# Optimization experiments

Measured on AMD Instinct MI355X. Metric: run time of the kernel, lower is better.

Reference implementation:

```python
import jax, jax.numpy as jnp
import numpy as np
from jax import lax

D_MODEL = 768
D_STATE = 64
D_CONV = 4
EXPAND = 2
HEADDIM = 64
D_INNER = EXPAND * D_MODEL          # 1536
NHEADS = D_INNER // HEADDIM          # 24
NGROUPS = 1
CONV_DIM = D_INNER + 2 * NGROUPS * D_STATE      # 1664
D_IN_PROJ = 2 * D_INNER + 2 * NGROUPS * D_STATE + NHEADS  # 3224
EPS = 1e-5


def setup_inputs() -> dict:
    key = jax.random.key(0)
    ks = jax.random.split(key, 8)
    B, L = 2, 4096
    x = jax.random.normal(ks[0], (B, L, D_MODEL), jnp.float32)
    W_in = jax.random.normal(ks[1], (D_MODEL, D_IN_PROJ), jnp.float32) * (D_MODEL ** -0.5)
    conv_w = jax.random.normal(ks[2], (CONV_DIM, D_CONV), jnp.float32) * 0.2
    conv_b = jnp.zeros((CONV_DIM,), jnp.float32)
    # dt_bias so that softplus(dt_bias) ~ [1e-3, 1e-1], like mamba init
    dt = jax.random.uniform(ks[3], (NHEADS,), jnp.float32, 1e-3, 1e-1)
    dt_bias = dt + jnp.log(-jnp.expm1(-dt))
    A_log = jnp.log(jax.random.uniform(ks[4], (NHEADS,), jnp.float32, 1.0, 16.0))
    D = jnp.ones((NHEADS,), jnp.float32)
    norm_w = jnp.ones((D_INNER,), jnp.float32)
    W_out = jax.random.normal(ks[5], (D_INNER, D_MODEL), jnp.float32) * (D_INNER ** -0.5)
    return {"x": x, "W_in": W_in, "conv_w": conv_w, "conv_b": conv_b,
            "dt_bias": dt_bias, "A_log": A_log, "D": D,
            "norm_w": norm_w, "W_out": W_out}


def _mamba2(x, W_in, conv_w, conv_b, dt_bias, A_log, D, norm_w, W_out):
    B, L, _ = x.shape
    zxbcdt = x @ W_in                                  # (B,L,3224)
    z = zxbcdt[..., :D_INNER]                          # gate
    xBC = zxbcdt[..., D_INNER:D_INNER + CONV_DIM]
    dt = zxbcdt[..., D_INNER + CONV_DIM:]              # (B,L,H)
    dt = jax.nn.softplus(dt + dt_bias)

    # causal depthwise conv1d, kernel D_CONV, then SiLU
    xp = jnp.pad(xBC, ((0, 0), (D_CONV - 1, 0), (0, 0)))
    conv = sum(xp[:, k:k + L, :] * conv_w[:, k] for k in range(D_CONV))
    xBC = jax.nn.silu(conv + conv_b)

    xs = xBC[..., :D_INNER].reshape(B, L, NHEADS, HEADDIM)
    Bm = xBC[..., D_INNER:D_INNER + D_STATE]           # (B,L,N)
    Cm = xBC[..., D_INNER + D_STATE:]                  # (B,L,N)

    A = -jnp.exp(A_log)                                # (H,)
    dA = jnp.exp(dt * A)                               # (B,L,H)

    def step(h, inp):
        dA_t, dt_t, x_t, B_t, C_t = inp
        # h: (B,H,P,N)
        h = h * dA_t[:, :, None, None] \
            + (dt_t[:, :, None] * x_t)[..., None] * B_t[:, None, None, :]
        y = jnp.einsum('bhpn,bn->bhp', h, C_t)
        return h, y

    inps = (jnp.moveaxis(dA, 1, 0), jnp.moveaxis(dt, 1, 0),
            jnp.moveaxis(xs, 1, 0), jnp.moveaxis(Bm, 1, 0),
            jnp.moveaxis(Cm, 1, 0))
    h0 = jnp.zeros((B, NHEADS, HEADDIM, D_STATE), x.dtype)
    _, ys = lax.scan(step, h0, inps)                   # (L,B,H,P)
    y = jnp.moveaxis(ys, 0, 1) + D[None, None, :, None] * xs
    y = y.reshape(B, L, D_INNER)

    # gated RMSNorm: norm(y * silu(z)) * norm_w
    y = y * jax.nn.silu(z)
    y = y * lax.rsqrt(jnp.mean(y * y, axis=-1, keepdims=True) + EPS) * norm_w
    return y @ W_out


def reference(x, W_in, conv_w, conv_b, dt_bias, A_log, D, norm_w, W_out):
    return _mamba2(x, W_in, conv_w, conv_b, dt_bias, A_log, D, norm_w, W_out)
```

## Files before the change

### kernel.cpp

```cpp
#include <hip/hip_runtime.h>

#define B_   2
#define L_   4096
#define DM   768
#define DI   1536
#define DS   64
#define H_   24
#define P_   64
#define CD   1664
#define NPJ  3224
#define N1   3200
#define Q_   64
#define NC   64
#define SP   76
#define HS   72
#define WDS  772
#define CROWS 16

typedef short          bf16x8 __attribute__((ext_vector_type(8)));
typedef _Float16       f16x8  __attribute__((ext_vector_type(8)));
typedef unsigned short us8    __attribute__((ext_vector_type(8)));
typedef unsigned short us4    __attribute__((ext_vector_type(4)));
typedef float          f32x4  __attribute__((ext_vector_type(4)));

__device__ __forceinline__ unsigned short f2bf(float f) {
  unsigned u = __float_as_uint(f);
  u += 0x7fffu + ((u >> 16) & 1u);
  return (unsigned short)(u >> 16);
}
__device__ __forceinline__ float bf2f(unsigned short u) {
  return __uint_as_float(((unsigned)u) << 16);
}
__device__ __forceinline__ float siluf(float x) { return x / (1.f + expf(-x)); }
__device__ __forceinline__ float softplusf(float x) { return (x > 20.f) ? x : log1pf(expf(x)); }

__device__ __forceinline__ void gload16(const unsigned short* g, unsigned short* l) {
  __builtin_amdgcn_global_load_lds(
      (const __attribute__((address_space(1))) void*)g,
      (__attribute__((address_space(3))) void*)l, 16, 0, 0);
}

__global__ __launch_bounds__(256)
void k_transpose_cast(const float* __restrict__ src, unsigned short* __restrict__ dst,
                      int R, int C)
{
  __shared__ float tile[32][33];
  const int tx = threadIdx.x & 31, ty = threadIdx.x >> 5;
  const int r0 = blockIdx.x * 32, c0 = blockIdx.y * 32;
#pragma unroll
  for (int r = 0; r < 4; ++r) {
    int rr = r0 + ty + r * 8, cc = c0 + tx;
    if (rr < R && cc < C) tile[ty + r * 8][tx] = src[(size_t)rr * C + cc];
  }
  __syncthreads();
#pragma unroll
  for (int r = 0; r < 4; ++r) {
    int orow = c0 + ty + r * 8, ocol = r0 + tx;
    if (orow < C && ocol < R) dst[(size_t)orow * R + ocol] = f2bf(tile[tx][ty + r * 8]);
  }
}

__global__ void k_wdtT(const float* __restrict__ W_in, float* __restrict__ WdtT)
{
  const int idx = blockIdx.x * 256 + threadIdx.x;
  if (idx >= H_ * DM) return;
  const int k = idx / H_, h = idx % H_;
  WdtT[(size_t)h * DM + k] = W_in[(size_t)k * NPJ + N1 + h];
}

template<int BM, int BN, int WM, int WN, bool OUT_BF16>
__global__ __launch_bounds__(256)
void k_gemm_t(const unsigned short* __restrict__ A, const unsigned short* __restrict__ Bt,
              void* __restrict__ C0v, int ld0, int ncol0,
              void* __restrict__ C1v, int ld1, int K)
{
  constexpr int MI = WM / 16, NI = WN / 16;
  constexpr int WAVES_N = BN / WN;
  constexpr int RA = BM / 32, RB = BN / 32;
  const int m0 = blockIdx.x * BM, n0 = blockIdx.y * BN;
  __shared__ unsigned short As[BM][64];
  __shared__ unsigned short Bs[BN][64];
  const int tid  = threadIdx.x;
  const int wave = tid >> 6, lane = tid & 63;
  const int quad = lane >> 4, r16 = lane & 15;
  const int wm = (wave / WAVES_N) * WM, wn = (wave % WAVES_N) * WN;

  const int lr8 = lane >> 3;
  const int csw = ((lane & 7) ^ lr8) * 8;
  const unsigned short* gA = A  + (size_t)(m0 + wave * 8 + lr8) * K + csw;
  const unsigned short* gB = Bt + (size_t)(n0 + wave * 8 + lr8) * K + csw;
  unsigned short* lA = &As[wave * 8][0] + (size_t)lane * 8;
  unsigned short* lB = &Bs[wave * 8][0] + (size_t)lane * 8;

  f32x4 acc[MI][NI];
#pragma unroll
  for (int mi = 0; mi < MI; ++mi)
#pragma unroll
    for (int ni = 0; ni < NI; ++ni) acc[mi][ni] = (f32x4){0.f, 0.f, 0.f, 0.f};

  for (int k0 = 0; k0 < K; k0 += 64) {
#pragma unroll
    for (int r = 0; r < RA; ++r)
      gload16(gA + (size_t)(r * 32) * K + k0, lA + (size_t)r * 32 * 64);
#pragma unroll
    for (int r = 0; r < RB; ++r)
      gload16(gB + (size_t)(r * 32) * K + k0, lB + (size_t)r * 32 * 64);
    __syncthreads();
    bf16x8 af[MI][2], bfr[NI][2];
#pragma unroll
    for (int mi = 0; mi < MI; ++mi)
#pragma unroll
      for (int ks = 0; ks < 2; ++ks)
        af[mi][ks] = *(const bf16x8*)&As[wm + mi * 16 + r16][((quad + ks * 4) ^ (r16 & 7)) * 8];
#pragma unroll
    for (int ni = 0; ni < NI; ++ni)
#pragma unroll
      for (int ks = 0; ks < 2; ++ks)
        bfr[ni][ks] = *(const bf16x8*)&Bs[wn + ni * 16 + r16][((quad + ks * 4) ^ (r16 & 7)) * 8];
#pragma unroll
    for (int mi = 0; mi < MI; ++mi)
#pragma unroll
      for (int ni = 0; ni < NI; ++ni)
#pragma unroll
        for (int ks = 0; ks < 2; ++ks)
          acc[mi][ni] = __builtin_amdgcn_mfma_f32_16x16x32_bf16(
              af[mi][ks], bfr[ni][ks], acc[mi][ni], 0, 0, 0);
    __syncthreads();
  }
#pragma unroll
  for (int mi = 0; mi < MI; ++mi)
#pragma unroll
    for (int ni = 0; ni < NI; ++ni) {
      int col = n0 + wn + ni * 16 + r16;
      void* dst; int ld, c;
      if (col < ncol0) { dst = C0v; ld = ld0; c = col; }
      else             { dst = C1v; ld = ld1; c = col - ncol0; }
#pragma unroll
      for (int r = 0; r < 4; ++r) {
        int row = m0 + wm + mi * 16 + quad * 4 + r;
        if (OUT_BF16) ((unsigned short*)dst)[(size_t)row * ld + c] = f2bf(acc[mi][ni][r]);
        else          ((float*)dst)[(size_t)row * ld + c] = acc[mi][ni][r];
      }
    }
}

__global__ __launch_bounds__(256)
void k_conv2(const unsigned short* __restrict__ xbc, const float* __restrict__ cw,
             const float* __restrict__ cb, _Float16* __restrict__ xs,
             float* __restrict__ Bm, float* __restrict__ Cm)
{
  const int ch = blockIdx.x * 256 + threadIdx.x;
  if (ch >= CD) return;
  const int r0 = blockIdx.y * CROWS;
  const float w0 = cw[ch * 4], w1 = cw[ch * 4 + 1], w2 = cw[ch * 4 + 2], w3 = cw[ch * 4 + 3];
  const float bias = cb[ch];
  float a, b, c;
  if ((r0 & (L_ - 1)) == 0) {
    a = 0.f; b = 0.f; c = 0.f;
  } else {
    a = bf2f(xbc[(size_t)(r0 - 3) * CD + ch]);
    b = bf2f(xbc[(size_t)(r0 - 2) * CD + ch]);
    c = bf2f(xbc[(size_t)(r0 - 1) * CD + ch]);
  }
#pragma unroll
  for (int i = 0; i < CROWS; ++i) {
    const int lr = r0 + i;
    float d = bf2f(xbc[(size_t)lr * CD + ch]);
    float v = siluf(bias + a * w0 + b * w1 + c * w2 + d * w3);
    a = b; b = c; c = d;
    if (ch < DI)           xs[(size_t)lr * DI + ch] = (_Float16)v;
    else if (ch < DI + DS) Bm[(size_t)lr * DS + (ch - DI)] = v;
    else                   Cm[(size_t)lr * DS + (ch - DI - DS)] = v;
  }
}

__global__ __launch_bounds__(192)
void k_dt2(const float* __restrict__ x, const float* __restrict__ WdtT,
           const float* __restrict__ dt_bias, float* __restrict__ dtv,
           unsigned short* __restrict__ xb)
{
  __shared__ float sW[H_][WDS];
  for (int i = threadIdx.x; i < H_ * DM; i += 192)
    sW[i / DM][i % DM] = WdtT[i];
  const int h = threadIdx.x % H_, rloc = threadIdx.x / H_;
  const int lrow = blockIdx.x * 8 + rloc;
  const float* xr = x + (size_t)lrow * DM;
  __syncthreads();
  float acc = 0.f;
#pragma unroll 8
  for (int k = 0; k < DM; k += 4) {
    f32x4 xv = *(const f32x4*)(xr + k);
    f32x4 wv = *(const f32x4*)&sW[h][k];
    acc += xv[0] * wv[0] + xv[1] * wv[1] + xv[2] * wv[2] + xv[3] * wv[3];
  }
  dtv[(size_t)lrow * H_ + h] = softplusf(acc + dt_bias[h]);
  const float* xi = xr + h * 32;
  unsigned short* xo = xb + (size_t)lrow * DM + h * 32;
#pragma unroll
  for (int j = 0; j < 32; j += 8) {
    f32x4 a = *(const f32x4*)(xi + j);
    f32x4 b = *(const f32x4*)(xi + j + 4);
    us8 o;
#pragma unroll
    for (int e = 0; e < 4; ++e) { o[e] = f2bf(a[e]); o[e + 4] = f2bf(b[e]); }
    *(us8*)(xo + j) = o;
  }
}

__global__ void k_cum(const float* __restrict__ dtv, const float* __restrict__ A_log,
                      float* __restrict__ cumA, int n)
{
  const int idx = blockIdx.x * 256 + threadIdx.x;
  if (idx >= n) return;
  const int c = idx % NC;
  const int h = (idx / NC) % H_;
  const int bz = idx / (NC * H_);
  const float A = -expf(A_log[h]);
  float cum = 0.f;
  const int rowbase = bz * L_ + c * Q_;
  float* outp = cumA + (size_t)idx * Q_;
  for (int i = 0; i < Q_; ++i) {
    cum += dtv[(size_t)(rowbase + i) * H_ + h] * A;
    outp[i] = cum;
  }
}

__global__ __launch_bounds__(256)
void k_intra(const _Float16* __restrict__ xs, const float* __restrict__ Bm,
             const float* __restrict__ Cm, const float* __restrict__ dtv,
             const float* __restrict__ cumA, _Float16* __restrict__ ytot,
             _Float16* __restrict__ Sbuf)
{
  const int c = blockIdx.x, h = blockIdx.y, bz = blockIdx.z;
  const int gidx = (bz * H_ + h) * NC + c;
  __shared__ _Float16 sCW[Q_][HS];
  __shared__ _Float16 sB [Q_][HS];
  __shared__ _Float16 sBT[Q_][HS];
  __shared__ _Float16 sXT[Q_][HS];
  __shared__ float scum[Q_], sdt[Q_];
  const int tid = threadIdx.x;
  const int rowbase = bz * L_ + c * Q_;

  {
    const int j = tid >> 2, s16 = (tid & 3) * 16;
    if (tid < Q_) {
      scum[tid] = cumA[(size_t)gidx * Q_ + tid];
      sdt[tid]  = dtv[(size_t)(rowbase + tid) * H_ + h];
    }
    const _Float16* xsrc = xs + (size_t)(rowbase + j) * DI + h * P_ + s16;
    f16x8 xv0 = *(const f16x8*)xsrc;
    f16x8 xv1 = *(const f16x8*)(xsrc + 8);
    f32x4 bv[4], cv[4];
    const float* bsrc = Bm + (size_t)(rowbase + j) * DS + s16;
    const float* csrc = Cm + (size_t)(rowbase + j) * DS + s16;
#pragma unroll
    for (int q = 0; q < 4; ++q) {
      bv[q] = *(const f32x4*)(bsrc + q * 4);
      cv[q] = *(const f32x4*)(csrc + q * 4);
    }
    __syncthreads();
    const float coef = expf(scum[Q_ - 1] - scum[j]) * sdt[j];
    union { f16x8 v; _Float16 e[8]; } pc[2], pb[2];
#pragma unroll
    for (int q = 0; q < 4; ++q)
#pragma unroll
      for (int e = 0; e < 4; ++e) {
        int o = q * 4 + e;
        pc[o >> 3].e[o & 7] = (_Float16)cv[q][e];
        pb[o >> 3].e[o & 7] = (_Float16)bv[q][e];
        sBT[s16 + o][j] = (_Float16)(bv[q][e] * coef);
        sXT[s16 + o][j] = (o < 8) ? xv0[o] : xv1[o - 8];
      }
    *(f16x8*)&sCW[j][s16]     = pc[0].v;
    *(f16x8*)&sCW[j][s16 + 8] = pc[1].v;
    *(f16x8*)&sB [j][s16]     = pb[0].v;
    *(f16x8*)&sB [j][s16 + 8] = pb[1].v;
  }
  __syncthreads();

  const int wave = tid >> 6, lane = tid & 63;
  const int quad = lane >> 4, r16 = lane & 15;
  const int i0 = wave * 16;
  const int irow = i0 + quad * 4;

  f32x4 g[4];
#pragma unroll
  for (int q = 0; q < 4; ++q) g[q] = (f32x4){0.f, 0.f, 0.f, 0.f};
#pragma unroll
  for (int ni = 0; ni < 4; ++ni) {
    if (ni <= wave) {
#pragma unroll
      for (int ks = 0; ks < 2; ++ks)
        g[ni] = __builtin_amdgcn_mfma_f32_16x16x32_f16(
            *(const f16x8*)&sCW[i0 + r16][ks * 32 + quad * 8],
            *(const f16x8*)&sB [ni * 16 + r16][ks * 32 + quad * 8], g[ni], 0, 0, 0);
    }
  }
  float wv[4][4];
#pragma unroll
  for (int ni = 0; ni < 4; ++ni)
#pragma unroll
    for (int r = 0; r < 4; ++r) {
      int i = irow + r, jcol = ni * 16 + r16;
      float v = 0.f;
      if (ni <= wave && jcol <= i)
        v = g[ni][r] * expf(scum[i] - scum[jcol]) * sdt[jcol];
      wv[ni][r] = v;
    }
  __syncthreads();
#pragma unroll
  for (int ni = 0; ni < 4; ++ni)
#pragma unroll
    for (int r = 0; r < 4; ++r)
      sCW[irow + r][ni * 16 + r16] = (_Float16)wv[ni][r];
  __syncthreads();

  f32x4 y[4];
#pragma unroll
  for (int q = 0; q < 4; ++q) y[q] = (f32x4){0.f, 0.f, 0.f, 0.f};
#pragma unroll
  for (int ni = 0; ni < 4; ++ni)
#pragma unroll
    for (int ks = 0; ks < 2; ++ks) {
      if (ks == 0 || wave >= 2)
        y[ni] = __builtin_amdgcn_mfma_f32_16x16x32_f16(
            *(const f16x8*)&sCW[i0 + r16][ks * 32 + quad * 8],
            *(const f16x8*)&sXT[ni * 16 + r16][ks * 32 + quad * 8], y[ni], 0, 0, 0);
    }
#pragma unroll
  for (int ni = 0; ni < 4; ++ni)
#pragma unroll
    for (int r = 0; r < 4; ++r)
      ytot[(size_t)(rowbase + irow + r) * DI + h * P_ + ni * 16 + r16] = (_Float16)y[ni][r];

  f32x4 t4[4];
#pragma unroll
  for (int q = 0; q < 4; ++q) t4[q] = (f32x4){0.f, 0.f, 0.f, 0.f};
#pragma unroll
  for (int ni = 0; ni < 4; ++ni)
#pragma unroll
    for (int ks = 0; ks < 2; ++ks)
      t4[ni] = __builtin_amdgcn_mfma_f32_16x16x32_f16(
          *(const f16x8*)&sBT[i0 + r16][ks * 32 + quad * 8],
          *(const f16x8*)&sXT[ni * 16 + r16][ks * 32 + quad * 8], t4[ni], 0, 0, 0);
  _Float16* sp = Sbuf + (size_t)gidx * (DS * P_);
#pragma unroll
  for (int ni = 0; ni < 4; ++ni)
#pragma unroll
    for (int r = 0; r < 4; ++r)
      sp[(irow + r) * P_ + ni * 16 + r16] = (_Float16)t4[ni][r];
}

__global__ void k_chunkscan(_Float16* __restrict__ Sbuf, const float* __restrict__ cumA)
{
  const int seg = blockIdx.x, h = blockIdx.y, bz = blockIdx.z;
  const int bh = bz * H_ + h;
  __shared__ float dec[NC];
  const int tid = threadIdx.x;
  if (tid < NC) dec[tid] = expf(cumA[((size_t)(bh * NC + tid)) * Q_ + (Q_ - 1)]);
  __syncthreads();
  const size_t off = (size_t)seg * 512 + (size_t)tid * 8;
  float s[8];
#pragma unroll
  for (int e = 0; e < 8; ++e) s[e] = 0.f;
  size_t base = (size_t)bh * NC * (DS * P_) + off;
  for (int c = 0; c < NC; ++c) {
    _Float16* p = Sbuf + base + (size_t)c * (DS * P_);
    f16x8 v = *(const f16x8*)p;
    f16x8 sto;
#pragma unroll
    for (int e = 0; e < 8; ++e) sto[e] = (_Float16)s[e];
    *(f16x8*)p = sto;
    const float d = dec[c];
#pragma unroll
    for (int e = 0; e < 8; ++e) s[e] = s[e] * d + (float)v[e];
  }
}

__global__ __launch_bounds__(256)
void k_inter(const _Float16* __restrict__ xs, const float* __restrict__ Cm,
             const float* __restrict__ cumA, const _Float16* __restrict__ Sbuf,
             const float* __restrict__ Dp, _Float16* __restrict__ ytot)
{
  const int c = blockIdx.x, h = blockIdx.y, bz = blockIdx.z;
  const int gidx = (bz * H_ + h) * NC + c;
  __shared__ float sS[DS][SP];
  __shared__ float sC[Q_][SP];
  __shared__ float scum[Q_];
  const int tid = threadIdx.x;
  const int jr = tid >> 2, blk = (tid & 3) * 16;
  const int rowbase = bz * L_ + c * Q_;
  {
    const _Float16* ssrc = Sbuf + (size_t)gidx * (DS * P_) + jr * P_ + blk;
    f16x8 sv0 = *(const f16x8*)ssrc;
    f16x8 sv1 = *(const f16x8*)(ssrc + 8);
    const float* csrc = Cm + (size_t)(rowbase + jr) * DS + blk;
#pragma unroll
    for (int o = 0; o < 8; ++o) {
      sS[jr][blk + o]     = (float)sv0[o];
      sS[jr][blk + 8 + o] = (float)sv1[o];
    }
#pragma unroll
    for (int q = 0; q < 4; ++q)
      *(f32x4*)&sC[jr][blk + q * 4] = *(const f32x4*)(csrc + q * 4);
    if (tid < Q_) scum[tid] = cumA[(size_t)gidx * Q_ + tid];
  }
  __syncthreads();
  const int i = jr;
  f32x4 acc[4];
#pragma unroll
  for (int q = 0; q < 4; ++q) acc[q] = (f32x4){0.f, 0.f, 0.f, 0.f};
  for (int n = 0; n < DS; ++n) {
    float cv = sC[i][n];
#pragma unroll
    for (int q = 0; q < 4; ++q) acc[q] += cv * *(const f32x4*)&sS[n][blk + q * 4];
  }
  const float e = expf(scum[i]);
  const float Dh = Dp[h];
  _Float16* yt = ytot + (size_t)(rowbase + i) * DI + h * P_ + blk;
  const _Float16* xsr = xs + (size_t)(rowbase + i) * DI + h * P_ + blk;
  f16x8 xa = *(const f16x8*)xsr;
  f16x8 xb2 = *(const f16x8*)(xsr + 8);
  f16x8 y0 = *(const f16x8*)yt;
  f16x8 y1 = *(const f16x8*)(yt + 8);
#pragma unroll
  for (int o = 0; o < 16; ++o) {
    float cur = (float)((o < 8) ? y0[o] : y1[o - 8]);
    float xf  = (float)((o < 8) ? xa[o] : xb2[o - 8]);
    cur += e * acc[o >> 2][o & 3] + Dh * xf;
    if (o < 8) y0[o] = (_Float16)cur; else y1[o - 8] = (_Float16)cur;
  }
  *(f16x8*)yt = y0;
  *(f16x8*)(yt + 8) = y1;
}

__global__ __launch_bounds__(192)
void k_rms(const unsigned short* __restrict__ z, const _Float16* __restrict__ ytot,
           const float* __restrict__ norm_w, unsigned short* __restrict__ ynorm)
{
  const int row = blockIdx.x, tid = threadIdx.x;
  const int e0 = tid * 8;
  us8 zv = *(const us8*)(z + (size_t)row * DI + e0);
  f16x8 yv = *(const f16x8*)(ytot + (size_t)row * DI + e0);
  float g[8];
  float ss = 0.f;
#pragma unroll
  for (int q = 0; q < 8; ++q) {
    g[q] = (float)yv[q] * siluf(bf2f(zv[q]));
    ss += g[q] * g[q];
  }
#pragma unroll
  for (int off = 32; off > 0; off >>= 1) ss += __shfl_down(ss, off);
  __shared__ float wsum[3];
  __shared__ float sscale;
  if ((tid & 63) == 0) wsum[tid >> 6] = ss;
  __syncthreads();
  if (tid == 0) sscale = rsqrtf((wsum[0] + wsum[1] + wsum[2]) * (1.f / DI) + 1e-5f);
  __syncthreads();
  const float sc = sscale;
  us8 o;
#pragma unroll
  for (int q = 0; q < 8; ++q) o[q] = f2bf(g[q] * sc * norm_w[e0 + q]);
  *(us8*)(ynorm + (size_t)row * DI + e0) = o;
}

extern "C" void kernel_launch(void* const* d_in, const int* in_sizes, int n_in,
                              void* d_out, int out_size, void* d_ws, size_t ws_size,
                              hipStream_t stream)
{
  (void)in_sizes; (void)n_in; (void)out_size;
  const float* x       = (const float*)d_in[0];
  const float* W_in    = (const float*)d_in[1];
  const float* conv_w  = (const float*)d_in[2];
  const float* conv_b  = (const float*)d_in[3];
  const float* dt_bias = (const float*)d_in[4];
  const float* A_log   = (const float*)d_in[5];
  const float* Dp      = (const float*)d_in[6];
  const float* norm_w  = (const float*)d_in[7];
  const float* W_out   = (const float*)d_in[8];
  float* out = (float*)d_out;

  const int nb = ((size_t)2 * L_ * 16320 + 7385088 <= ws_size) ? 2 : 1;
  const int rows = nb * L_;

  char* ws = (char*)d_ws;
  unsigned short* zseg = (unsigned short*)ws;  ws += (size_t)rows * DI * 2;
  unsigned short* xbc  = (unsigned short*)ws;  ws += (size_t)rows * CD * 2;
  _Float16* xs   = (_Float16*)ws;  ws += (size_t)rows * DI * 2;
  _Float16* ytot = (_Float16*)ws;  ws += (size_t)rows * DI * 2;
  float* Bm   = (float*)ws;  ws += (size_t)rows * DS * 4;
  float* Cm   = (float*)ws;  ws += (size_t)rows * DS * 4;
  float* dtv  = (float*)ws;  ws += (size_t)rows * H_ * 4;
  float* cumA = (float*)ws;  ws += (size_t)rows * H_ * 4;
  _Float16* Sbuf = (_Float16*)ws;  ws += (size_t)rows * 3072;
  unsigned short* WinT  = (unsigned short*)ws; ws += (size_t)NPJ * DM * 2;
  unsigned short* WoutT = (unsigned short*)ws; ws += (size_t)DM * DI * 2;
  float* WdtT   = (float*)ws;  ws += (size_t)H_ * DM * 4;
  unsigned short* xb    = (unsigned short*)Sbuf;
  unsigned short* ynorm = (unsigned short*)xs;

  k_transpose_cast<<<dim3(24, (NPJ + 31) / 32), 256, 0, stream>>>(W_in, WinT, DM, NPJ);
  k_transpose_cast<<<dim3(48, 24), 256, 0, stream>>>(W_out, WoutT, DI, DM);
  k_wdtT<<<(H_ * DM + 255) / 256, 256, 0, stream>>>(W_in, WdtT);

  for (int b0 = 0; b0 < B_; b0 += nb) {
    const float* xp = x + (size_t)b0 * L_ * DM;

    k_dt2<<<rows / 8, 192, 0, stream>>>(xp, WdtT, dt_bias, dtv, xb);
    k_gemm_t<128, 128, 64, 64, true><<<dim3(rows / 128, N1 / 128), 256, 0, stream>>>(
        xb, WinT, zseg, DI, DI, xbc, CD, DM);
    k_conv2<<<dim3(7, rows / CROWS), 256, 0, stream>>>(xbc, conv_w, conv_b, xs, Bm, Cm);
    k_cum<<<(nb * H_ * NC + 255) / 256, 256, 0, stream>>>(dtv, A_log, cumA, nb * H_ * NC);
    k_intra<<<dim3(NC, H_, nb), 256, 0, stream>>>(xs, Bm, Cm, dtv, cumA, ytot, Sbuf);
    k_chunkscan<<<dim3(8, H_, nb), 64, 0, stream>>>(Sbuf, cumA);
    k_inter<<<dim3(NC, H_, nb), 256, 0, stream>>>(xs, Cm, cumA, Sbuf, Dp, ytot);
    k_rms<<<rows, 192, 0, stream>>>(zseg, ytot, norm_w, ynorm);
    k_gemm_t<128, 64, 64, 32, false><<<dim3(rows / 128, DM / 64), 256, 0, stream>>>(
        ynorm, WoutT, out + (size_t)b0 * L_ * DM, DM, DM, out + (size_t)b0 * L_ * DM, DM, DI);
  }
}
```

Baseline: 342.9 us.

## Fuse cumsum into chunk kernels, store B/C in fp16, retile GEMMs

Removes the separate k_cum kernel and its cumA buffer: k_intra and k_inter now compute the per-chunk decay prefix sum with a wave-level shuffle scan, and k_intra writes the chunk-end decay that k_chunkscan needs. Bm/Cm are stored as fp16 instead of fp32, which halves their traffic. The in_proj GEMM writes into a single unified zx buffer and uses a larger 256x128 tile. The out_proj GEMM uses a 128-wide K step with a generalized swizzled load. These changes cut launches and memory traffic, but the larger tiles raise LDS and register pressure, and the fp16 B/C lose some precision.

```diff
diff --git a/kernel.cpp b/kernel.cpp
--- a/kernel.cpp
+++ b/kernel.cpp
@@ -20,7 +20,6 @@
 typedef short          bf16x8 __attribute__((ext_vector_type(8)));
 typedef _Float16       f16x8  __attribute__((ext_vector_type(8)));
 typedef unsigned short us8    __attribute__((ext_vector_type(8)));
-typedef unsigned short us4    __attribute__((ext_vector_type(4)));
 typedef float          f32x4  __attribute__((ext_vector_type(4)));
 
 __device__ __forceinline__ unsigned short f2bf(float f) {
@@ -68,29 +67,26 @@
   WdtT[(size_t)h * DM + k] = W_in[(size_t)k * NPJ + N1 + h];
 }
 
-template<int BM, int BN, int WM, int WN, bool OUT_BF16>
+template<int BM, int BN, int WM, int WN, int BK, bool OUT_BF16>
 __global__ __launch_bounds__(256)
 void k_gemm_t(const unsigned short* __restrict__ A, const unsigned short* __restrict__ Bt,
-              void* __restrict__ C0v, int ld0, int ncol0,
-              void* __restrict__ C1v, int ld1, int K)
-{
-  constexpr int MI = WM / 16, NI = WN / 16;
+              void* __restrict__ Cv, int ldc, int K)
+{
+  constexpr int MI = WM / 16, NI = WN / 16, KS = BK / 32;
   constexpr int WAVES_N = BN / WN;
-  constexpr int RA = BM / 32, RB = BN / 32;
+  constexpr int RPC = (BK == 64) ? 8 : 4;
+  constexpr int CPC = 64 / RPC;
+  constexpr int RA = BM / (4 * RPC), RB = BN / (4 * RPC);
   const int m0 = blockIdx.x * BM, n0 = blockIdx.y * BN;
-  __shared__ unsigned short As[BM][64];
-  __shared__ unsigned short Bs[BN][64];
+  __shared__ unsigned short As[BM][BK];
+  __shared__ unsigned short Bs[BN][BK];
   const int tid  = threadIdx.x;
   const int wave = tid >> 6, lane = tid & 63;
   const int quad = lane >> 4, r16 = lane & 15;
   const int wm = (wave / WAVES_N) * WM, wn = (wave % WAVES_N) * WN;
 
-  const int lr8 = lane >> 3;
-  const int csw = ((lane & 7) ^ lr8) * 8;
-  const unsigned short* gA = A  + (size_t)(m0 + wave * 8 + lr8) * K + csw;
-  const unsigned short* gB = Bt + (size_t)(n0 + wave * 8 + lr8) * K + csw;
-  unsigned short* lA = &As[wave * 8][0] + (size_t)lane * 8;
-  unsigned short* lB = &Bs[wave * 8][0] + (size_t)lane * 8;
+  const int lrr = lane / CPC;
+  const int lcc = lane % CPC;
 
   f32x4 acc[MI][NI];
 #pragma unroll
@@ -98,59 +94,62 @@
 #pragma unroll
     for (int ni = 0; ni < NI; ++ni) acc[mi][ni] = (f32x4){0.f, 0.f, 0.f, 0.f};
 
-  for (int k0 = 0; k0 < K; k0 += 64) {
-#pragma unroll
-    for (int r = 0; r < RA; ++r)
-      gload16(gA + (size_t)(r * 32) * K + k0, lA + (size_t)r * 32 * 64);
-#pragma unroll
-    for (int r = 0; r < RB; ++r)
-      gload16(gB + (size_t)(r * 32) * K + k0, lB + (size_t)r * 32 * 64);
+  for (int k0 = 0; k0 < K; k0 += BK) {
+#pragma unroll
+    for (int r = 0; r < RA; ++r) {
+      const int row = r * 4 * RPC + wave * RPC + lrr;
+      const int csw = ((lcc ^ (row & 7)) * 8);
+      gload16(A + (size_t)(m0 + row) * K + k0 + csw,
+              &As[r * 4 * RPC + wave * RPC][0] + (size_t)lane * 8);
+    }
+#pragma unroll
+    for (int r = 0; r < RB; ++r) {
+      const int row = r * 4 * RPC + wave * RPC + lrr;
+      const int csw = ((lcc ^ (row & 7)) * 8);
+      gload16(Bt + (size_t)(n0 + row) * K + k0 + csw,
+              &Bs[r * 4 * RPC + wave * RPC][0] + (size_t)lane * 8);
+    }
     __syncthreads();
-    bf16x8 af[MI][2], bfr[NI][2];
-#pragma unroll
-    for (int mi = 0; mi < MI; ++mi)
-#pragma unroll
-      for (int ks = 0; ks < 2; ++ks)
-        af[mi][ks] = *(const bf16x8*)&As[wm + mi * 16 + r16][((quad + ks * 4) ^ (r16 & 7)) * 8];
-#pragma unroll
-    for (int ni = 0; ni < NI; ++ni)
-#pragma unroll
-      for (int ks = 0; ks < 2; ++ks)
-        bfr[ni][ks] = *(const bf16x8*)&Bs[wn + ni * 16 + r16][((quad + ks * 4) ^ (r16 & 7)) * 8];
-#pragma unroll
-    for (int mi = 0; mi < MI; ++mi)
+#pragma unroll
+    for (int ks = 0; ks < KS; ++ks) {
+      bf16x8 af[MI], bfr[NI];
+#pragma unroll
+      for (int mi = 0; mi < MI; ++mi)
+        af[mi] = *(const bf16x8*)&As[wm + mi * 16 + r16][((quad + ks * 4) ^ (r16 & 7)) * 8];
 #pragma unroll
       for (int ni = 0; ni < NI; ++ni)
-#pragma unroll
-        for (int ks = 0; ks < 2; ++ks)
+        bfr[ni] = *(const bf16x8*)&Bs[wn + ni * 16 + r16][((quad + ks * 4) ^ (r16 & 7)) * 8];
+#pragma unroll
+      for (int mi = 0; mi < MI; ++mi)
+#pragma unroll
+        for (int ni = 0; ni < NI; ++ni)
           acc[mi][ni] = __builtin_amdgcn_mfma_f32_16x16x32_bf16(
-              af[mi][ks], bfr[ni][ks], acc[mi][ni], 0, 0, 0);
+              af[mi], bfr[ni], acc[mi][ni], 0, 0, 0);
+    }
     __syncthreads();
   }
 #pragma unroll
   for (int mi = 0; mi < MI; ++mi)
 #pragma unroll
     for (int ni = 0; ni < NI; ++ni) {
-      int col = n0 + wn + ni * 16 + r16;
-      void* dst; int ld, c;
-      if (col < ncol0) { dst = C0v; ld = ld0; c = col; }
-      else             { dst = C1v; ld = ld1; c = col - ncol0; }
+      const int col = n0 + wn + ni * 16 + r16;
 #pragma unroll
       for (int r = 0; r < 4; ++r) {
-        int row = m0 + wm + mi * 16 + quad * 4 + r;
-        if (OUT_BF16) ((unsigned short*)dst)[(size_t)row * ld + c] = f2bf(acc[mi][ni][r]);
-        else          ((float*)dst)[(size_t)row * ld + c] = acc[mi][ni][r];
+        const int row = m0 + wm + mi * 16 + quad * 4 + r;
+        if (OUT_BF16) ((unsigned short*)Cv)[(size_t)row * ldc + col] = f2bf(acc[mi][ni][r]);
+        else          ((float*)Cv)[(size_t)row * ldc + col] = acc[mi][ni][r];
       }
     }
 }
 
 __global__ __launch_bounds__(256)
-void k_conv2(const unsigned short* __restrict__ xbc, const float* __restrict__ cw,
+void k_conv2(const unsigned short* __restrict__ zx, const float* __restrict__ cw,
              const float* __restrict__ cb, _Float16* __restrict__ xs,
-             float* __restrict__ Bm, float* __restrict__ Cm)
+             _Float16* __restrict__ Bm, _Float16* __restrict__ Cm)
 {
   const int ch = blockIdx.x * 256 + threadIdx.x;
   if (ch >= CD) return;
+  const unsigned short* xbc = zx + DI;
   const int r0 = blockIdx.y * CROWS;
   const float w0 = cw[ch * 4], w1 = cw[ch * 4 + 1], w2 = cw[ch * 4 + 2], w3 = cw[ch * 4 + 3];
   const float bias = cb[ch];
@@ -158,19 +157,19 @@
   if ((r0 & (L_ - 1)) == 0) {
     a = 0.f; b = 0.f; c = 0.f;
   } else {
-    a = bf2f(xbc[(size_t)(r0 - 3) * CD + ch]);
-    b = bf2f(xbc[(size_t)(r0 - 2) * CD + ch]);
-    c = bf2f(xbc[(size_t)(r0 - 1) * CD + ch]);
+    a = bf2f(xbc[(size_t)(r0 - 3) * N1 + ch]);
+    b = bf2f(xbc[(size_t)(r0 - 2) * N1 + ch]);
+    c = bf2f(xbc[(size_t)(r0 - 1) * N1 + ch]);
   }
 #pragma unroll
   for (int i = 0; i < CROWS; ++i) {
     const int lr = r0 + i;
-    float d = bf2f(xbc[(size_t)lr * CD + ch]);
+    float d = bf2f(xbc[(size_t)lr * N1 + ch]);
     float v = siluf(bias + a * w0 + b * w1 + c * w2 + d * w3);
     a = b; b = c; c = d;
     if (ch < DI)           xs[(size_t)lr * DI + ch] = (_Float16)v;
-    else if (ch < DI + DS) Bm[(size_t)lr * DS + (ch - DI)] = v;
-    else                   Cm[(size_t)lr * DS + (ch - DI - DS)] = v;
+    else if (ch < DI + DS) Bm[(size_t)lr * DS + (ch - DI)] = (_Float16)v;
+    else                   Cm[(size_t)lr * DS + (ch - DI - DS)] = (_Float16)v;
   }
 }
 
@@ -207,29 +206,11 @@
   }
 }
 
-__global__ void k_cum(const float* __restrict__ dtv, const float* __restrict__ A_log,
-                      float* __restrict__ cumA, int n)
-{
-  const int idx = blockIdx.x * 256 + threadIdx.x;
-  if (idx >= n) return;
-  const int c = idx % NC;
-  const int h = (idx / NC) % H_;
-  const int bz = idx / (NC * H_);
-  const float A = -expf(A_log[h]);
-  float cum = 0.f;
-  const int rowbase = bz * L_ + c * Q_;
-  float* outp = cumA + (size_t)idx * Q_;
-  for (int i = 0; i < Q_; ++i) {
-    cum += dtv[(size_t)(rowbase + i) * H_ + h] * A;
-    outp[i] = cum;
-  }
-}
-
 __global__ __launch_bounds__(256)
-void k_intra(const _Float16* __restrict__ xs, const float* __restrict__ Bm,
-             const float* __restrict__ Cm, const float* __restrict__ dtv,
-             const float* __restrict__ cumA, _Float16* __restrict__ ytot,
-             _Float16* __restrict__ Sbuf)
+void k_intra(const _Float16* __restrict__ xs, const _Float16* __restrict__ Bm,
+             const _Float16* __restrict__ Cm, const float* __restrict__ dtv,
+             const float* __restrict__ A_log, _Float16* __restrict__ ytot,
+             _Float16* __restrict__ Sbuf, float* __restrict__ decb)
 {
   const int c = blockIdx.x, h = blockIdx.y, bz = blockIdx.z;
   const int gidx = (bz * H_ + h) * NC + c;
@@ -244,37 +225,39 @@
   {
     const int j = tid >> 2, s16 = (tid & 3) * 16;
     if (tid < Q_) {
-      scum[tid] = cumA[(size_t)gidx * Q_ + tid];
-      sdt[tid]  = dtv[(size_t)(rowbase + tid) * H_ + h];
+      float ld = dtv[(size_t)(rowbase + tid) * H_ + h];
+      sdt[tid] = ld;
+      const float A = -expf(A_log[h]);
+      float v = ld * A;
+#pragma unroll
+      for (int off = 1; off < 64; off <<= 1) {
+        float n = __shfl_up(v, off, 64);
+        if (tid >= off) v += n;
+      }
+      scum[tid] = v;
+      if (tid == Q_ - 1) decb[gidx] = expf(v);
     }
     const _Float16* xsrc = xs + (size_t)(rowbase + j) * DI + h * P_ + s16;
     f16x8 xv0 = *(const f16x8*)xsrc;
     f16x8 xv1 = *(const f16x8*)(xsrc + 8);
-    f32x4 bv[4], cv[4];
-    const float* bsrc = Bm + (size_t)(rowbase + j) * DS + s16;
-    const float* csrc = Cm + (size_t)(rowbase + j) * DS + s16;
-#pragma unroll
-    for (int q = 0; q < 4; ++q) {
-      bv[q] = *(const f32x4*)(bsrc + q * 4);
-      cv[q] = *(const f32x4*)(csrc + q * 4);
-    }
+    const _Float16* bsrc = Bm + (size_t)(rowbase + j) * DS + s16;
+    const _Float16* csrc = Cm + (size_t)(rowbase + j) * DS + s16;
+    f16x8 bv0 = *(const f16x8*)bsrc;
+    f16x8 bv1 = *(const f16x8*)(bsrc + 8);
+    f16x8 cv0 = *(const f16x8*)csrc;
+    f16x8 cv1 = *(const f16x8*)(csrc + 8);
     __syncthreads();
     const float coef = expf(scum[Q_ - 1] - scum[j]) * sdt[j];
-    union { f16x8 v; _Float16 e[8]; } pc[2], pb[2];
-#pragma unroll
-    for (int q = 0; q < 4; ++q)
-#pragma unroll
-      for (int e = 0; e < 4; ++e) {
-        int o = q * 4 + e;
-        pc[o >> 3].e[o & 7] = (_Float16)cv[q][e];
-        pb[o >> 3].e[o & 7] = (_Float16)bv[q][e];
-        sBT[s16 + o][j] = (_Float16)(bv[q][e] * coef);
-        sXT[s16 + o][j] = (o < 8) ? xv0[o] : xv1[o - 8];
-      }
-    *(f16x8*)&sCW[j][s16]     = pc[0].v;
-    *(f16x8*)&sCW[j][s16 + 8] = pc[1].v;
-    *(f16x8*)&sB [j][s16]     = pb[0].v;
-    *(f16x8*)&sB [j][s16 + 8] = pb[1].v;
+#pragma unroll
+    for (int o = 0; o < 16; ++o) {
+      _Float16 bh = (o < 8) ? bv0[o] : bv1[o - 8];
+      sBT[s16 + o][j] = (_Float16)((float)bh * coef);
+      sXT[s16 + o][j] = (o < 8) ? xv0[o] : xv1[o - 8];
+    }
+    *(f16x8*)&sCW[j][s16]     = cv0;
+    *(f16x8*)&sCW[j][s16 + 8] = cv1;
+    *(f16x8*)&sB [j][s16]     = bv0;
+    *(f16x8*)&sB [j][s16 + 8] = bv1;
   }
   __syncthreads();
 
@@ -351,13 +334,13 @@
       sp[(irow + r) * P_ + ni * 16 + r16] = (_Float16)t4[ni][r];
 }
 
-__global__ void k_chunkscan(_Float16* __restrict__ Sbuf, const float* __restrict__ cumA)
+__global__ void k_chunkscan(_Float16* __restrict__ Sbuf, const float* __restrict__ decb)
 {
   const int seg = blockIdx.x, h = blockIdx.y, bz = blockIdx.z;
   const int bh = bz * H_ + h;
   __shared__ float dec[NC];
   const int tid = threadIdx.x;
-  if (tid < NC) dec[tid] = expf(cumA[((size_t)(bh * NC + tid)) * Q_ + (Q_ - 1)]);
+  if (tid < NC) dec[tid] = decb[bh * NC + tid];
   __syncthreads();
   const size_t off = (size_t)seg * 512 + (size_t)tid * 8;
   float s[8];
@@ -378,32 +361,42 @@
 }
 
 __global__ __launch_bounds__(256)
-void k_inter(const _Float16* __restrict__ xs, const float* __restrict__ Cm,
-             const float* __restrict__ cumA, const _Float16* __restrict__ Sbuf,
-             const float* __restrict__ Dp, _Float16* __restrict__ ytot)
+void k_inter(const _Float16* __restrict__ xs, const _Float16* __restrict__ Cm,
+             const float* __restrict__ dtv, const float* __restrict__ A_log,
+             const _Float16* __restrict__ Sbuf, const float* __restrict__ Dp,
+             _Float16* __restrict__ ytot)
 {
   const int c = blockIdx.x, h = blockIdx.y, bz = blockIdx.z;
   const int gidx = (bz * H_ + h) * NC + c;
   __shared__ float sS[DS][SP];
   __shared__ float sC[Q_][SP];
-  __shared__ float scum[Q_];
+  __shared__ float escum[Q_];
   const int tid = threadIdx.x;
   const int jr = tid >> 2, blk = (tid & 3) * 16;
   const int rowbase = bz * L_ + c * Q_;
   {
+    if (tid < Q_) {
+      float v = dtv[(size_t)(rowbase + tid) * H_ + h] * (-expf(A_log[h]));
+#pragma unroll
+      for (int off = 1; off < 64; off <<= 1) {
+        float n = __shfl_up(v, off, 64);
+        if (tid >= off) v += n;
+      }
+      escum[tid] = expf(v);
+    }
     const _Float16* ssrc = Sbuf + (size_t)gidx * (DS * P_) + jr * P_ + blk;
     f16x8 sv0 = *(const f16x8*)ssrc;
     f16x8 sv1 = *(const f16x8*)(ssrc + 8);
-    const float* csrc = Cm + (size_t)(rowbase + jr) * DS + blk;
+    const _Float16* csrc = Cm + (size_t)(rowbase + jr) * DS + blk;
+    f16x8 cv0 = *(const f16x8*)csrc;
+    f16x8 cv1 = *(const f16x8*)(csrc + 8);
 #pragma unroll
     for (int o = 0; o < 8; ++o) {
       sS[jr][blk + o]     = (float)sv0[o];
       sS[jr][blk + 8 + o] = (float)sv1[o];
-    }
-#pragma unroll
-    for (int q = 0; q < 4; ++q)
-      *(f32x4*)&sC[jr][blk + q * 4] = *(const f32x4*)(csrc + q * 4);
-    if (tid < Q_) scum[tid] = cumA[(size_t)gidx * Q_ + tid];
+      sC[jr][blk + o]     = (float)cv0[o];
+      sC[jr][blk + 8 + o] = (float)cv1[o];
+    }
   }
   __syncthreads();
   const int i = jr;
@@ -415,7 +408,7 @@
 #pragma unroll
     for (int q = 0; q < 4; ++q) acc[q] += cv * *(const f32x4*)&sS[n][blk + q * 4];
   }
-  const float e = expf(scum[i]);
+  const float e = escum[i];
   const float Dh = Dp[h];
   _Float16* yt = ytot + (size_t)(rowbase + i) * DI + h * P_ + blk;
   const _Float16* xsr = xs + (size_t)(rowbase + i) * DI + h * P_ + blk;
@@ -435,12 +428,12 @@
 }
 
 __global__ __launch_bounds__(192)
-void k_rms(const unsigned short* __restrict__ z, const _Float16* __restrict__ ytot,
+void k_rms(const unsigned short* __restrict__ zx, const _Float16* __restrict__ ytot,
            const float* __restrict__ norm_w, unsigned short* __restrict__ ynorm)
 {
   const int row = blockIdx.x, tid = threadIdx.x;
   const int e0 = tid * 8;
-  us8 zv = *(const us8*)(z + (size_t)row * DI + e0);
+  us8 zv = *(const us8*)(zx + (size_t)row * N1 + e0);
   f16x8 yv = *(const f16x8*)(ytot + (size_t)row * DI + e0);
   float g[8];
   float ss = 0.f;
@@ -480,22 +473,21 @@
   const float* W_out   = (const float*)d_in[8];
   float* out = (float*)d_out;
 
-  const int nb = ((size_t)2 * L_ * 16320 + 7385088 <= ws_size) ? 2 : 1;
+  const int nb = ((size_t)2 * L_ * 15968 + 14737408 <= ws_size) ? 2 : 1;
   const int rows = nb * L_;
 
   char* ws = (char*)d_ws;
-  unsigned short* zseg = (unsigned short*)ws;  ws += (size_t)rows * DI * 2;
-  unsigned short* xbc  = (unsigned short*)ws;  ws += (size_t)rows * CD * 2;
+  unsigned short* zx = (unsigned short*)ws;  ws += (size_t)rows * N1 * 2;
   _Float16* xs   = (_Float16*)ws;  ws += (size_t)rows * DI * 2;
   _Float16* ytot = (_Float16*)ws;  ws += (size_t)rows * DI * 2;
-  float* Bm   = (float*)ws;  ws += (size_t)rows * DS * 4;
-  float* Cm   = (float*)ws;  ws += (size_t)rows * DS * 4;
+  _Float16* Bm   = (_Float16*)ws;  ws += (size_t)rows * DS * 2;
+  _Float16* Cm   = (_Float16*)ws;  ws += (size_t)rows * DS * 2;
   float* dtv  = (float*)ws;  ws += (size_t)rows * H_ * 4;
-  float* cumA = (float*)ws;  ws += (size_t)rows * H_ * 4;
   _Float16* Sbuf = (_Float16*)ws;  ws += (size_t)rows * 3072;
   unsigned short* WinT  = (unsigned short*)ws; ws += (size_t)NPJ * DM * 2;
   unsigned short* WoutT = (unsigned short*)ws; ws += (size_t)DM * DI * 2;
-  float* WdtT   = (float*)ws;  ws += (size_t)H_ * DM * 4;
+  float* WdtT = (float*)ws;  ws += (size_t)H_ * DM * 4;
+  float* decb = (float*)ws;  ws += (size_t)nb * H_ * NC * 4;
   unsigned short* xb    = (unsigned short*)Sbuf;
   unsigned short* ynorm = (unsigned short*)xs;
 
@@ -507,15 +499,14 @@
     const float* xp = x + (size_t)b0 * L_ * DM;
 
     k_dt2<<<rows / 8, 192, 0, stream>>>(xp, WdtT, dt_bias, dtv, xb);
-    k_gemm_t<128, 128, 64, 64, true><<<dim3(rows / 128, N1 / 128), 256, 0, stream>>>(
-        xb, WinT, zseg, DI, DI, xbc, CD, DM);
-    k_conv2<<<dim3(7, rows / CROWS), 256, 0, stream>>>(xbc, conv_w, conv_b, xs, Bm, Cm);
-    k_cum<<<(nb * H_ * NC + 255) / 256, 256, 0, stream>>>(dtv, A_log, cumA, nb * H_ * NC);
-    k_intra<<<dim3(NC, H_, nb), 256, 0, stream>>>(xs, Bm, Cm, dtv, cumA, ytot, Sbuf);
-    k_chunkscan<<<dim3(8, H_, nb), 64, 0, stream>>>(Sbuf, cumA);
-    k_inter<<<dim3(NC, H_, nb), 256, 0, stream>>>(xs, Cm, cumA, Sbuf, Dp, ytot);
-    k_rms<<<rows, 192, 0, stream>>>(zseg, ytot, norm_w, ynorm);
-    k_gemm_t<128, 64, 64, 32, false><<<dim3(rows / 128, DM / 64), 256, 0, stream>>>(
-        ynorm, WoutT, out + (size_t)b0 * L_ * DM, DM, DM, out + (size_t)b0 * L_ * DM, DM, DI);
-  }
-}
+    k_gemm_t<256, 128, 128, 64, 64, true><<<dim3(rows / 256, N1 / 128), 256, 0, stream>>>(
+        xb, WinT, zx, N1, DM);
+    k_conv2<<<dim3(7, rows / CROWS), 256, 0, stream>>>(zx, conv_w, conv_b, xs, Bm, Cm);
+    k_intra<<<dim3(NC, H_, nb), 256, 0, stream>>>(xs, Bm, Cm, dtv, A_log, ytot, Sbuf, decb);
+    k_chunkscan<<<dim3(8, H_, nb), 64, 0, stream>>>(Sbuf, decb);
+    k_inter<<<dim3(NC, H_, nb), 256, 0, stream>>>(xs, Cm, dtv, A_log, Sbuf, Dp, ytot);
+    k_rms<<<rows, 192, 0, stream>>>(zx, ytot, norm_w, ynorm);
+    k_gemm_t<128, 64, 64, 32, 128, false><<<dim3(rows / 128, DM / 64), 256, 0, stream>>>(
+        ynorm, WoutT, out + (size_t)b0 * L_ * DM, DM, DI);
+  }
+}
```

Result: slower. 362.7 us (+5.8%).
